# Kernel tuning notes

Hardware: AMD Instinct MI355X
Metric: run time of the kernel (lower is better)

## Reference

```python
import jax, jax.numpy as jnp
import numpy as np

B, N, DIM = 2, 2048, 512
HEADS, DIM_HEAD = 8, 64
INNER = HEADS * DIM_HEAD  # 512
SCALE = DIM_HEAD ** -0.5


def setup_inputs() -> dict:
    key = jax.random.key(0)
    k1, k2, k3, k4, k5 = jax.random.split(key, 5)
    s = 0.02
    return {
        "x1": jax.random.normal(k1, (B, N, DIM), jnp.float32),
        "x2": jax.random.normal(k2, (B, N, DIM), jnp.float32),
        "W_qk": jax.random.normal(k3, (DIM, 2 * INNER), jnp.float32) * s,
        "W_v": jax.random.normal(k4, (DIM, INNER), jnp.float32) * s,
        "W_out": jax.random.normal(k5, (INNER, DIM), jnp.float32) * s,
        "b_out": jnp.zeros((DIM,), jnp.float32),
    }


def _split_heads(t):
    # [b, n, h*d] -> [b, h, n, d]
    b, n, _ = t.shape
    return t.reshape(b, n, HEADS, DIM_HEAD).transpose(0, 2, 1, 3)


def reference(x1, x2, W_qk, W_v, W_out, b_out):
    # to_qk(x1) -> chunk into k, v ; to_v(x2) -> q  (names in orig are swapped)
    kv = x1 @ W_qk                      # [b, n1, 2*inner]
    k, v = jnp.split(kv, 2, axis=-1)
    q = x2 @ W_v                        # [b, n2, inner]
    q, k, v = _split_heads(q), _split_heads(k), _split_heads(v)  # [b,h,n,d]
    dots = jnp.einsum("bhid,bhjd->bhij", q, k) * SCALE  # [b,h,n2,n1]
    attn = jax.nn.softmax(dots, axis=-1)
    out = jnp.einsum("bhij,bhjd->bhid", attn, v)         # [b,h,n2,d]
    out = out.transpose(0, 2, 1, 3).reshape(out.shape[0], out.shape[2], INNER)
    return out @ W_out + b_out          # [b, n2, dim]
```

## Files before the change

### kernel.cpp

```cpp
#include <hip/hip_runtime.h>

typedef short bf16x8 __attribute__((ext_vector_type(8)));
typedef short bf16x4 __attribute__((ext_vector_type(4)));
typedef float f32x4 __attribute__((ext_vector_type(4)));
typedef float f32x16 __attribute__((ext_vector_type(16)));
typedef unsigned short u16;
typedef unsigned int u32;
typedef u16 u16x8 __attribute__((ext_vector_type(8)));
typedef u16 u16x4 __attribute__((ext_vector_type(4)));

#define DEV __device__ __forceinline__

DEV u16 f2bf(float f) {
  unsigned u = __float_as_uint(f);
  u += 0x7fff + ((u >> 16) & 1);
  return (u16)(u >> 16);
}

DEV int pkbf(float lo, float hi) {
  return __builtin_amdgcn_perm(__float_as_uint(hi) + 0x8000u,
                               __float_as_uint(lo) + 0x8000u, 0x07060302u);
}

#define MFMA16(a, b, c) __builtin_amdgcn_mfma_f32_16x16x32_bf16(a, b, c, 0, 0, 0)
#define MFMA3216(a, b, c) __builtin_amdgcn_mfma_f32_32x32x16_bf16(a, b, c, 0, 0, 0)

#if __has_builtin(__builtin_amdgcn_mfma_f32_32x32x8bf16_1k)
#define HAVE_PV8 1
#define PVMFMA(a, b, c) __builtin_amdgcn_mfma_f32_32x32x8bf16_1k(a, b, c, 0, 0, 0)
#else
#define HAVE_PV8 0
#endif

#if __has_builtin(__builtin_amdgcn_exp2f)
#define QSCALE 0.18033688011112042f
#define EXPFN(x) __builtin_amdgcn_exp2f(x)
#else
#define QSCALE 0.125f
#define EXPFN(x) __expf(x)
#endif

#define GLD16(gp, lp)                                                     \
  __builtin_amdgcn_global_load_lds(                                       \
      (const __attribute__((address_space(1))) u32*)(gp),                 \
      (__attribute__((address_space(3))) u32*)(lp), 16, 0, 0)

__global__ __launch_bounds__(256) void wprep(
    const float* __restrict__ Wqk, const float* __restrict__ Wv,
    const float* __restrict__ Wout,
    const float* __restrict__ x1, const float* __restrict__ x2,
    u16* __restrict__ WqkT, u16* __restrict__ WvT, u16* __restrict__ WoutT,
    u16* __restrict__ x1b, u16* __restrict__ x2b) {
  __shared__ float tf[32][33];
  int bx = blockIdx.x, t = threadIdx.x;
  if (bx >= 1024) {
    int id = bx - 1024;
    const float* src = id < 1024 ? x1 : x2;
    u16* dst = id < 1024 ? x1b : x2b;
    long base = (long)(id & 1023) * 2048 + t * 8;
    float4 f0 = *(const float4*)(src + base);
    float4 f1 = *(const float4*)(src + base + 4);
    u16x8 o;
    o[0] = f2bf(f0.x); o[1] = f2bf(f0.y); o[2] = f2bf(f0.z); o[3] = f2bf(f0.w);
    o[4] = f2bf(f1.x); o[5] = f2bf(f1.y); o[6] = f2bf(f1.z); o[7] = f2bf(f1.w);
    *(u16x8*)(dst + base) = o;
    return;
  }
  const float* src; u16* dst; int Ncols; int id;
  if (bx < 512)      { id = bx;       src = Wqk;  dst = WqkT;  Ncols = 1024; }
  else if (bx < 768) { id = bx - 512; src = Wv;   dst = WvT;   Ncols = 512; }
  else               { id = bx - 768; src = Wout; dst = WoutT; Ncols = 512; }
  int tilesPerRow = Ncols >> 5;
  int tr = id / tilesPerRow, tc = id % tilesPerRow;
  int r0 = tr * 32, c0 = tc * 32;
  {
    int r = t >> 3, c4 = (t & 7) * 4;
    float4 v = *(const float4*)(src + (long)(r0 + r) * Ncols + c0 + c4);
    tf[r][c4] = v.x; tf[r][c4 + 1] = v.y; tf[r][c4 + 2] = v.z; tf[r][c4 + 3] = v.w;
  }
  __syncthreads();
  {
    int c = t >> 3, r4 = (t & 7) * 4;
    u16x4 o;
    o[0] = f2bf(tf[r4][c]); o[1] = f2bf(tf[r4 + 1][c]);
    o[2] = f2bf(tf[r4 + 2][c]); o[3] = f2bf(tf[r4 + 3][c]);
    *(u16x4*)(dst + (long)(c0 + c) * 512 + r0 + r4) = o;
  }
}

__global__ __launch_bounds__(256) void qkv_gemm(
    const u16* __restrict__ x1b, const u16* __restrict__ x2b,
    const u16* __restrict__ WqkT, const u16* __restrict__ WvT,
    u16* __restrict__ out_q, u16* __restrict__ out_k, u16* __restrict__ out_vt) {
  __shared__ u16 sA[2][128 * 40];
  __shared__ u16 sB[2][64 * 40];
  int bx = blockIdx.x, t = threadIdx.x;
  bool isQ = bx < 256;
  int bx2 = isQ ? bx : bx - 256;
  const u16* Ap = isQ ? x2b : x1b;
  const u16* BT = isQ ? WvT : WqkT;
  int m0 = (bx2 & 31) * 128, n0 = (bx2 >> 5) * 64;
  int w = t >> 6, l = t & 63, lm = l & 15, lq = l >> 4;

  f32x4 zero = {0.f, 0.f, 0.f, 0.f};
  f32x4 acc[2][4];
#pragma unroll
  for (int i = 0; i < 2; ++i)
#pragma unroll
    for (int j = 0; j < 4; ++j) acc[i][j] = zero;

  int sm = t >> 2;
  int skc = (t & 3) * 8;
  const u16* gA = Ap + (long)(m0 + sm) * 512 + skc;
  const u16* gB = BT + (long)(n0 + sm) * 512 + skc;

  bf16x8 a0 = *(const bf16x8*)(gA);
  bf16x8 a1 = *(const bf16x8*)(gA + 64 * 512);
  bf16x8 b0 = *(const bf16x8*)(gB);
  *(bf16x8*)(sA[0] + sm * 40 + skc) = a0;
  *(bf16x8*)(sA[0] + (sm + 64) * 40 + skc) = a1;
  *(bf16x8*)(sB[0] + sm * 40 + skc) = b0;
  __syncthreads();

  for (int kt = 0; kt < 16; ++kt) {
    int cur = kt & 1;
    if (kt < 15) {
      a0 = *(const bf16x8*)(gA + (kt + 1) * 32);
      a1 = *(const bf16x8*)(gA + 64 * 512 + (kt + 1) * 32);
      b0 = *(const bf16x8*)(gB + (kt + 1) * 32);
    }
    bf16x8 af[2], bfr[4];
    af[0] = *(const bf16x8*)(sA[cur] + (w * 32 + lm) * 40 + lq * 8);
    af[1] = *(const bf16x8*)(sA[cur] + (w * 32 + 16 + lm) * 40 + lq * 8);
#pragma unroll
    for (int s = 0; s < 4; ++s)
      bfr[s] = *(const bf16x8*)(sB[cur] + (s * 16 + lm) * 40 + lq * 8);
#pragma unroll
    for (int ms = 0; ms < 2; ++ms)
#pragma unroll
      for (int s = 0; s < 4; ++s)
        acc[ms][s] = MFMA16(af[ms], bfr[s], acc[ms][s]);
    if (kt < 15) {
      int nxt = 1 - cur;
      *(bf16x8*)(sA[nxt] + sm * 40 + skc) = a0;
      *(bf16x8*)(sA[nxt] + (sm + 64) * 40 + skc) = a1;
      *(bf16x8*)(sB[nxt] + sm * 40 + skc) = b0;
    }
    __syncthreads();
  }

#pragma unroll
  for (int ms = 0; ms < 2; ++ms) {
    int gmBase = m0 + w * 32 + ms * 16 + lq * 4;
#pragma unroll
    for (int s = 0; s < 4; ++s) {
      int gc = n0 + s * 16 + lm;
      int b = gmBase >> 11, n = gmBase & 2047;
      if (isQ) {
#pragma unroll
        for (int r = 0; r < 4; ++r)
          out_q[(((long)(b << 3) + (gc >> 6)) * 2048 + n + r) * 64 + (gc & 63)] =
              f2bf(acc[ms][s][r] * QSCALE);
      } else if (gc < 512) {
#pragma unroll
        for (int r = 0; r < 4; ++r)
          out_k[(((long)(b << 3) + (gc >> 6)) * 2048 + n + r) * 64 + (gc & 63)] =
              f2bf(acc[ms][s][r]);
      } else {
        int c = gc - 512, h = c >> 6, d = c & 63;
        u16x4 vv;
#pragma unroll
        for (int r = 0; r < 4; ++r) vv[r] = f2bf(acc[ms][s][r]);
        *(u16x4*)(out_vt + (((long)(b << 3) + h) * 64 + d) * 2048 + n) = vv;
      }
    }
  }
}

__global__ __launch_bounds__(256, 2) void attn(
    const u16* __restrict__ Q, const u16* __restrict__ K,
    const u16* __restrict__ Vt, u16* __restrict__ O) {
  int id = blockIdx.x;
  int bh = id & 15, qt = id >> 4;
  int b = bh >> 3, h = bh & 7;
  const u16* Kh = K + (long)bh * 2048 * 64;
  const u16* Vh = Vt + (long)bh * 64 * 2048;
  int t = threadIdx.x, w = t >> 6, lane = t & 63, ln = lane & 31, hi = lane >> 5;
  int g = w & 1, kh = w >> 1;

  __shared__ u16 smem[2][2][2][4096];

  bf16x8 qf[4];
  {
    const u16* qp = Q + (long)bh * 2048 * 64 + (long)(qt * 64 + g * 32 + ln) * 64 + hi * 8;
#pragma unroll
    for (int dc = 0; dc < 4; ++dc) qf[dc] = *(const bf16x8*)(qp + dc * 16);
  }

  f32x16 accO[2];
#pragma unroll
  for (int dt = 0; dt < 2; ++dt)
#pragma unroll
    for (int i = 0; i < 16; ++i) accO[dt][i] = 0.f;
  float dacc = 0.f;

  int lrow = lane >> 3;
  int swz = ((lane & 7) ^ lrow) * 8;
  const u16* gKl = Kh + (long)(kh * 1024 + g * 32 + lrow) * 64 + swz;
  const u16* gVl = Vh + (long)(g * 32 + lrow) * 2048 + kh * 1024 + swz;

  auto stage = [&](int jt, int buf) {
    u16* sK = smem[buf][0][kh];
    u16* sV = smem[buf][1][kh];
    const u16* gk = gKl + (long)jt * 4096;
    const u16* gv = gVl + jt * 64;
#pragma unroll
    for (int i = 0; i < 4; ++i) {
      GLD16(gk + i * 512, sK + (g * 32 + i * 8) * 64);
      GLD16(gv + (long)i * 16384, sV + (g * 32 + i * 8) * 64);
    }
  };

  stage(0, 0);
  __syncthreads();

  int swl = ln & 7;
  for (int jt = 0; jt < 16; ++jt) {
    int cur = jt & 1;
    if (jt < 15) stage(jt + 1, cur ^ 1);
    const u16* sKh = smem[cur][0][kh];
    const u16* sVh = smem[cur][1][kh];
#pragma unroll
    for (int kt2 = 0; kt2 < 2; ++kt2) {
      int rowK = (kt2 * 32 + ln) * 64;
      f32x16 st1, st2;
#pragma unroll
      for (int i = 0; i < 16; ++i) { st1[i] = 0.f; st2[i] = 0.f; }
      bf16x8 kf0 = *(const bf16x8*)(sKh + rowK + ((0 * 2 + hi) ^ swl) * 8);
      bf16x8 kf1 = *(const bf16x8*)(sKh + rowK + ((1 * 2 + hi) ^ swl) * 8);
      bf16x8 kf2 = *(const bf16x8*)(sKh + rowK + ((2 * 2 + hi) ^ swl) * 8);
      bf16x8 kf3 = *(const bf16x8*)(sKh + rowK + ((3 * 2 + hi) ^ swl) * 8);
      st1 = MFMA3216(kf0, qf[0], st1);
      st2 = MFMA3216(kf1, qf[1], st2);
      st1 = MFMA3216(kf2, qf[2], st1);
      st2 = MFMA3216(kf3, qf[3], st2);
      float p[16];
#pragma unroll
      for (int i = 0; i < 16; ++i) {
        float e = EXPFN(st1[i] + st2[i]);
        p[i] = e;
        dacc += e;
      }
#if HAVE_PV8
#pragma unroll
      for (int c = 0; c < 4; ++c) {
        union { int2 i2; bf16x4 v; } u;
        u.i2.x = pkbf(p[c * 4 + 0], p[c * 4 + 1]);
        u.i2.y = pkbf(p[c * 4 + 2], p[c * 4 + 3]);
#pragma unroll
        for (int dt = 0; dt < 2; ++dt) {
          bf16x4 vf = *(const bf16x4*)(sVh + (dt * 32 + ln) * 64 +
                                       (((kt2 * 4 + c) ^ swl) * 8) + hi * 4);
          accO[dt] = PVMFMA(vf, u.v, accO[dt]);
        }
      }
#else
#pragma unroll
      for (int c2 = 0; c2 < 2; ++c2) {
        int o0x = pkbf(p[c2 * 8 + 0], p[c2 * 8 + 1]);
        int o0y = pkbf(p[c2 * 8 + 2], p[c2 * 8 + 3]);
        int o1x = pkbf(p[c2 * 8 + 4], p[c2 * 8 + 5]);
        int o1y = pkbf(p[c2 * 8 + 6], p[c2 * 8 + 7]);
        int s0x = __shfl_xor(o0x, 32), s0y = __shfl_xor(o0y, 32);
        int s1x = __shfl_xor(o1x, 32), s1y = __shfl_xor(o1y, 32);
        union { int4 i4; bf16x8 v; } u;
        if (hi) { u.i4.x = s1x; u.i4.y = s1y; u.i4.z = o1x; u.i4.w = o1y; }
        else    { u.i4.x = o0x; u.i4.y = o0y; u.i4.z = s0x; u.i4.w = s0y; }
#pragma unroll
        for (int dt = 0; dt < 2; ++dt) {
          bf16x8 vf = *(const bf16x8*)(sVh + (dt * 32 + ln) * 64 +
                                       (((kt2 * 4 + c2 * 2 + hi) ^ swl) * 8));
          accO[dt] = MFMA3216(vf, u.v, accO[dt]);
        }
      }
#endif
    }
    __syncthreads();
  }

  float* cb = (float*)&smem[0][0][0][0];
  float* base = cb + g * 2112;
  if (kh == 1) {
#pragma unroll
    for (int dt = 0; dt < 2; ++dt)
#pragma unroll
      for (int i = 0; i < 16; ++i)
        base[(dt * 16 + i) * 64 + hi * 32 + ln] = accO[dt][i];
    base[2048 + hi * 32 + ln] = dacc;
  }
  __syncthreads();
  if (kh == 0) {
#pragma unroll
    for (int dt = 0; dt < 2; ++dt)
#pragma unroll
      for (int i = 0; i < 16; ++i)
        accO[dt][i] += base[(dt * 16 + i) * 64 + hi * 32 + ln];
    dacc += base[2048 + hi * 32 + ln];
    dacc += __shfl_xor(dacc, 32);
    float inv = 1.f / dacc;

    u16* Ob = O + ((long)b * 2048 + qt * 64 + g * 32 + ln) * 512 + h * 64;
#pragma unroll
    for (int dt = 0; dt < 2; ++dt)
#pragma unroll
      for (int gq = 0; gq < 4; ++gq) {
        u16x4 o;
#pragma unroll
        for (int rr = 0; rr < 4; ++rr) o[rr] = f2bf(accO[dt][gq * 4 + rr] * inv);
        *(u16x4*)(Ob + dt * 32 + gq * 8 + hi * 4) = o;
      }
  }
}

__global__ __launch_bounds__(128) void out_gemm(
    const u16* __restrict__ A, const u16* __restrict__ BT,
    float* __restrict__ out_f, const float* __restrict__ bias) {
  __shared__ u16 sA[2][64 * 40];
  __shared__ u16 sB[2][32 * 40];
  int t = threadIdx.x, bx = blockIdx.x;
  int m0 = (bx & 63) * 64, n0 = (bx >> 6) * 32;
  int w = t >> 6, l = t & 63, lm = l & 15, lq = l >> 4;

  f32x4 zero = {0.f, 0.f, 0.f, 0.f};
  f32x4 acc[2][2];
#pragma unroll
  for (int i = 0; i < 2; ++i)
#pragma unroll
    for (int j = 0; j < 2; ++j) acc[i][j] = zero;

  int ar = t >> 1, akc = (t & 1) * 16;
  int br = t >> 2, bkc = (t & 3) * 8;
  const u16* gA = A + (long)(m0 + ar) * 512 + akc;
  const u16* gB = BT + (long)(n0 + br) * 512 + bkc;

  bf16x8 a0 = *(const bf16x8*)(gA);
  bf16x8 a1 = *(const bf16x8*)(gA + 8);
  bf16x8 b0 = *(const bf16x8*)(gB);
  *(bf16x8*)(sA[0] + ar * 40 + akc) = a0;
  *(bf16x8*)(sA[0] + ar * 40 + akc + 8) = a1;
  *(bf16x8*)(sB[0] + br * 40 + bkc) = b0;
  __syncthreads();

  for (int kt = 0; kt < 16; ++kt) {
    int cur = kt & 1;
    if (kt < 15) {
      a0 = *(const bf16x8*)(gA + (kt + 1) * 32);
      a1 = *(const bf16x8*)(gA + (kt + 1) * 32 + 8);
      b0 = *(const bf16x8*)(gB + (kt + 1) * 32);
    }
    bf16x8 af[2], bfr[2];
    af[0] = *(const bf16x8*)(sA[cur] + (w * 32 + lm) * 40 + lq * 8);
    af[1] = *(const bf16x8*)(sA[cur] + (w * 32 + 16 + lm) * 40 + lq * 8);
    bfr[0] = *(const bf16x8*)(sB[cur] + (lm)*40 + lq * 8);
    bfr[1] = *(const bf16x8*)(sB[cur] + (16 + lm) * 40 + lq * 8);
#pragma unroll
    for (int ms = 0; ms < 2; ++ms)
#pragma unroll
      for (int s = 0; s < 2; ++s)
        acc[ms][s] = MFMA16(af[ms], bfr[s], acc[ms][s]);
    if (kt < 15) {
      int nxt = 1 - cur;
      *(bf16x8*)(sA[nxt] + ar * 40 + akc) = a0;
      *(bf16x8*)(sA[nxt] + ar * 40 + akc + 8) = a1;
      *(bf16x8*)(sB[nxt] + br * 40 + bkc) = b0;
    }
    __syncthreads();
  }

#pragma unroll
  for (int ms = 0; ms < 2; ++ms) {
    int gmBase = m0 + w * 32 + ms * 16 + lq * 4;
#pragma unroll
    for (int s = 0; s < 2; ++s) {
      int gc = n0 + s * 16 + lm;
      float bv = bias[gc];
#pragma unroll
      for (int r = 0; r < 4; ++r)
        out_f[(long)(gmBase + r) * 512 + gc] = acc[ms][s][r] + bv;
    }
  }
}

extern "C" void kernel_launch(void* const* d_in, const int* in_sizes, int n_in,
                              void* d_out, int out_size, void* d_ws, size_t ws_size,
                              hipStream_t stream) {
  const float* x1 = (const float*)d_in[0];
  const float* x2 = (const float*)d_in[1];
  const float* Wqk = (const float*)d_in[2];
  const float* Wv = (const float*)d_in[3];
  const float* Wout = (const float*)d_in[4];
  const float* bout = (const float*)d_in[5];
  float* out = (float*)d_out;

  u16* ws = (u16*)d_ws;
  const long SZ = 2097152;
  u16* Qw = ws;
  u16* Kw = ws + SZ;
  u16* Vtw = ws + 2 * SZ;
  u16* Ow = ws + 3 * SZ;
  u16* WqkT = ws + 4 * SZ;
  u16* WvT = WqkT + 524288;
  u16* WoutT = WvT + 262144;
  u16* x1b = WoutT + 262144;
  u16* x2b = x1b + SZ;

  wprep<<<3072, 256, 0, stream>>>(Wqk, Wv, Wout, x1, x2, WqkT, WvT, WoutT, x1b, x2b);
  qkv_gemm<<<768, 256, 0, stream>>>(x1b, x2b, WqkT, WvT, Qw, Kw, Vtw);
  attn<<<512, 256, 0, stream>>>(Qw, Kw, Vtw, Ow);
  out_gemm<<<1024, 128, 0, stream>>>(Ow, WoutT, out, bout);
}
```

Before: 126.6 us.

## Use 128x128 GEMM tiles with direct global-to-LDS swizzled loads and MFMA priority hints

The QKV and output projection GEMMs move to 128x128 tiles with a 2x2 wave layout. Operands are staged straight from global memory into LDS through GLD16 with an XOR swizzle instead of register round-trips through padded arrays. The larger tiles raise operand reuse and shrink the grids (384 and 128 blocks), at the cost of fewer blocks to fill the CUs. The attention kernel also gets s_setprio around its MFMA sections and a tree-shaped sum for the softmax denominator.

```diff
diff --git a/kernel.cpp b/kernel.cpp
--- a/kernel.cpp
+++ b/kernel.cpp
@@ -92,70 +92,70 @@
     const u16* __restrict__ x1b, const u16* __restrict__ x2b,
     const u16* __restrict__ WqkT, const u16* __restrict__ WvT,
     u16* __restrict__ out_q, u16* __restrict__ out_k, u16* __restrict__ out_vt) {
-  __shared__ u16 sA[2][128 * 40];
-  __shared__ u16 sB[2][64 * 40];
+  __shared__ u16 sA[2][128 * 32];
+  __shared__ u16 sB[2][128 * 32];
   int bx = blockIdx.x, t = threadIdx.x;
-  bool isQ = bx < 256;
-  int bx2 = isQ ? bx : bx - 256;
+  bool isQ = bx < 128;
+  int bx2 = isQ ? bx : bx - 128;
   const u16* Ap = isQ ? x2b : x1b;
   const u16* BT = isQ ? WvT : WqkT;
-  int m0 = (bx2 & 31) * 128, n0 = (bx2 >> 5) * 64;
+  int m0 = (bx2 & 31) * 128, n0 = (bx2 >> 5) * 128;
   int w = t >> 6, l = t & 63, lm = l & 15, lq = l >> 4;
+  int wr = w >> 1, wc = w & 1;
 
   f32x4 zero = {0.f, 0.f, 0.f, 0.f};
-  f32x4 acc[2][4];
-#pragma unroll
-  for (int i = 0; i < 2; ++i)
+  f32x4 acc[4][4];
+#pragma unroll
+  for (int i = 0; i < 4; ++i)
 #pragma unroll
     for (int j = 0; j < 4; ++j) acc[i][j] = zero;
 
-  int sm = t >> 2;
-  int skc = (t & 3) * 8;
-  const u16* gA = Ap + (long)(m0 + sm) * 512 + skc;
-  const u16* gB = BT + (long)(n0 + sm) * 512 + skc;
-
-  bf16x8 a0 = *(const bf16x8*)(gA);
-  bf16x8 a1 = *(const bf16x8*)(gA + 64 * 512);
-  bf16x8 b0 = *(const bf16x8*)(gB);
-  *(bf16x8*)(sA[0] + sm * 40 + skc) = a0;
-  *(bf16x8*)(sA[0] + (sm + 64) * 40 + skc) = a1;
-  *(bf16x8*)(sB[0] + sm * 40 + skc) = b0;
+  int srow = w * 16 + (l >> 2);
+  int swzk = ((l & 3) ^ ((l >> 3) & 3)) * 8;
+  const u16* gAsrc = Ap + (long)(m0 + srow) * 512 + swzk;
+  const u16* gBsrc = BT + (long)(n0 + srow) * 512 + swzk;
+
+  auto stage = [&](int kt, int buf) {
+    const u16* a0 = gAsrc + kt * 32;
+    const u16* b0 = gBsrc + kt * 32;
+    GLD16(a0,            sA[buf] + w * 512);
+    GLD16(a0 + 64 * 512, sA[buf] + 2048 + w * 512);
+    GLD16(b0,            sB[buf] + w * 512);
+    GLD16(b0 + 64 * 512, sB[buf] + 2048 + w * 512);
+  };
+
+  stage(0, 0);
   __syncthreads();
+
+  int rchunk = (lq ^ ((lm >> 1) & 3)) * 8;
+  int frA = (wr * 64 + lm) * 32 + rchunk;
+  int frB = (wc * 64 + lm) * 32 + rchunk;
 
   for (int kt = 0; kt < 16; ++kt) {
     int cur = kt & 1;
-    if (kt < 15) {
-      a0 = *(const bf16x8*)(gA + (kt + 1) * 32);
-      a1 = *(const bf16x8*)(gA + 64 * 512 + (kt + 1) * 32);
-      b0 = *(const bf16x8*)(gB + (kt + 1) * 32);
-    }
-    bf16x8 af[2], bfr[4];
-    af[0] = *(const bf16x8*)(sA[cur] + (w * 32 + lm) * 40 + lq * 8);
-    af[1] = *(const bf16x8*)(sA[cur] + (w * 32 + 16 + lm) * 40 + lq * 8);
+    if (kt < 15) stage(kt + 1, cur ^ 1);
+    bf16x8 af[4], bfr[4];
+#pragma unroll
+    for (int ms = 0; ms < 4; ++ms)
+      af[ms] = *(const bf16x8*)(sA[cur] + frA + ms * 512);
 #pragma unroll
     for (int s = 0; s < 4; ++s)
-      bfr[s] = *(const bf16x8*)(sB[cur] + (s * 16 + lm) * 40 + lq * 8);
-#pragma unroll
-    for (int ms = 0; ms < 2; ++ms)
+      bfr[s] = *(const bf16x8*)(sB[cur] + frB + s * 512);
+#pragma unroll
+    for (int ms = 0; ms < 4; ++ms)
 #pragma unroll
       for (int s = 0; s < 4; ++s)
         acc[ms][s] = MFMA16(af[ms], bfr[s], acc[ms][s]);
-    if (kt < 15) {
-      int nxt = 1 - cur;
-      *(bf16x8*)(sA[nxt] + sm * 40 + skc) = a0;
-      *(bf16x8*)(sA[nxt] + (sm + 64) * 40 + skc) = a1;
-      *(bf16x8*)(sB[nxt] + sm * 40 + skc) = b0;
-    }
     __syncthreads();
   }
 
 #pragma unroll
-  for (int ms = 0; ms < 2; ++ms) {
-    int gmBase = m0 + w * 32 + ms * 16 + lq * 4;
+  for (int ms = 0; ms < 4; ++ms) {
+    int gmBase = m0 + wr * 64 + ms * 16 + lq * 4;
+    int b = gmBase >> 11, n = gmBase & 2047;
 #pragma unroll
     for (int s = 0; s < 4; ++s) {
-      int gc = n0 + s * 16 + lm;
-      int b = gmBase >> 11, n = gmBase & 2047;
+      int gc = n0 + wc * 64 + s * 16 + lm;
       if (isQ) {
 #pragma unroll
         for (int r = 0; r < 4; ++r)
@@ -240,18 +240,22 @@
       bf16x8 kf1 = *(const bf16x8*)(sKh + rowK + ((1 * 2 + hi) ^ swl) * 8);
       bf16x8 kf2 = *(const bf16x8*)(sKh + rowK + ((2 * 2 + hi) ^ swl) * 8);
       bf16x8 kf3 = *(const bf16x8*)(sKh + rowK + ((3 * 2 + hi) ^ swl) * 8);
+      __builtin_amdgcn_s_setprio(1);
       st1 = MFMA3216(kf0, qf[0], st1);
       st2 = MFMA3216(kf1, qf[1], st2);
       st1 = MFMA3216(kf2, qf[2], st1);
       st2 = MFMA3216(kf3, qf[3], st2);
+      __builtin_amdgcn_s_setprio(0);
       float p[16];
 #pragma unroll
-      for (int i = 0; i < 16; ++i) {
-        float e = EXPFN(st1[i] + st2[i]);
-        p[i] = e;
-        dacc += e;
-      }
+      for (int i = 0; i < 16; ++i) p[i] = EXPFN(st1[i] + st2[i]);
+      float q0 = (p[0] + p[1]) + (p[2] + p[3]);
+      float q1 = (p[4] + p[5]) + (p[6] + p[7]);
+      float q2 = (p[8] + p[9]) + (p[10] + p[11]);
+      float q3 = (p[12] + p[13]) + (p[14] + p[15]);
+      dacc += (q0 + q1) + (q2 + q3);
 #if HAVE_PV8
+      __builtin_amdgcn_s_setprio(1);
 #pragma unroll
       for (int c = 0; c < 4; ++c) {
         union { int2 i2; bf16x4 v; } u;
@@ -264,7 +268,9 @@
           accO[dt] = PVMFMA(vf, u.v, accO[dt]);
         }
       }
+      __builtin_amdgcn_s_setprio(0);
 #else
+      __builtin_amdgcn_s_setprio(1);
 #pragma unroll
       for (int c2 = 0; c2 < 2; ++c2) {
         int o0x = pkbf(p[c2 * 8 + 0], p[c2 * 8 + 1]);
@@ -283,6 +289,7 @@
           accO[dt] = MFMA3216(vf, u.v, accO[dt]);
         }
       }
+      __builtin_amdgcn_s_setprio(0);
 #endif
     }
     __syncthreads();
@@ -322,71 +329,72 @@
   }
 }
 
-__global__ __launch_bounds__(128) void out_gemm(
+__global__ __launch_bounds__(256) void out_gemm(
     const u16* __restrict__ A, const u16* __restrict__ BT,
     float* __restrict__ out_f, const float* __restrict__ bias) {
-  __shared__ u16 sA[2][64 * 40];
-  __shared__ u16 sB[2][32 * 40];
-  int t = threadIdx.x, bx = blockIdx.x;
-  int m0 = (bx & 63) * 64, n0 = (bx >> 6) * 32;
+  __shared__ u16 sA[2][128 * 32];
+  __shared__ u16 sB[2][128 * 32];
+  int bx = blockIdx.x, t = threadIdx.x;
+  int m0 = (bx & 31) * 128, n0 = (bx >> 5) * 128;
   int w = t >> 6, l = t & 63, lm = l & 15, lq = l >> 4;
+  int wr = w >> 1, wc = w & 1;
 
   f32x4 zero = {0.f, 0.f, 0.f, 0.f};
-  f32x4 acc[2][2];
-#pragma unroll
-  for (int i = 0; i < 2; ++i)
-#pragma unroll
-    for (int j = 0; j < 2; ++j) acc[i][j] = zero;
-
-  int ar = t >> 1, akc = (t & 1) * 16;
-  int br = t >> 2, bkc = (t & 3) * 8;
-  const u16* gA = A + (long)(m0 + ar) * 512 + akc;
-  const u16* gB = BT + (long)(n0 + br) * 512 + bkc;
-
-  bf16x8 a0 = *(const bf16x8*)(gA);
-  bf16x8 a1 = *(const bf16x8*)(gA + 8);
-  bf16x8 b0 = *(const bf16x8*)(gB);
-  *(bf16x8*)(sA[0] + ar * 40 + akc) = a0;
-  *(bf16x8*)(sA[0] + ar * 40 + akc + 8) = a1;
-  *(bf16x8*)(sB[0] + br * 40 + bkc) = b0;
+  f32x4 acc[4][4];
+#pragma unroll
+  for (int i = 0; i < 4; ++i)
+#pragma unroll
+    for (int j = 0; j < 4; ++j) acc[i][j] = zero;
+
+  int srow = w * 16 + (l >> 2);
+  int swzk = ((l & 3) ^ ((l >> 3) & 3)) * 8;
+  const u16* gAsrc = A + (long)(m0 + srow) * 512 + swzk;
+  const u16* gBsrc = BT + (long)(n0 + srow) * 512 + swzk;
+
+  auto stage = [&](int kt, int buf) {
+    const u16* a0 = gAsrc + kt * 32;
+    const u16* b0 = gBsrc + kt * 32;
+    GLD16(a0,            sA[buf] + w * 512);
+    GLD16(a0 + 64 * 512, sA[buf] + 2048 + w * 512);
+    GLD16(b0,            sB[buf] + w * 512);
+    GLD16(b0 + 64 * 512, sB[buf] + 2048 + w * 512);
+  };
+
+  stage(0, 0);
   __syncthreads();
+
+  int rchunk = (lq ^ ((lm >> 1) & 3)) * 8;
+  int frA = (wr * 64 + lm) * 32 + rchunk;
+  int frB = (wc * 64 + lm) * 32 + rchunk;
 
   for (int kt = 0; kt < 16; ++kt) {
     int cur = kt & 1;
-    if (kt < 15) {
-      a0 = *(const bf16x8*)(gA + (kt + 1) * 32);
-      a1 = *(const bf16x8*)(gA + (kt + 1) * 32 + 8);
-      b0 = *(const bf16x8*)(gB + (kt + 1) * 32);
-    }
-    bf16x8 af[2], bfr[2];
-    af[0] = *(const bf16x8*)(sA[cur] + (w * 32 + lm) * 40 + lq * 8);
-    af[1] = *(const bf16x8*)(sA[cur] + (w * 32 + 16 + lm) * 40 + lq * 8);
-    bfr[0] = *(const bf16x8*)(sB[cur] + (lm)*40 + lq * 8);
-    bfr[1] = *(const bf16x8*)(sB[cur] + (16 + lm) * 40 + lq * 8);
-#pragma unroll
-    for (int ms = 0; ms < 2; ++ms)
-#pragma unroll
-      for (int s = 0; s < 2; ++s)
+    if (kt < 15) stage(kt + 1, cur ^ 1);
+    bf16x8 af[4], bfr[4];
+#pragma unroll
+    for (int ms = 0; ms < 4; ++ms)
+      af[ms] = *(const bf16x8*)(sA[cur] + frA + ms * 512);
+#pragma unroll
+    for (int s = 0; s < 4; ++s)
+      bfr[s] = *(const bf16x8*)(sB[cur] + frB + s * 512);
+#pragma unroll
+    for (int ms = 0; ms < 4; ++ms)
+#pragma unroll
+      for (int s = 0; s < 4; ++s)
         acc[ms][s] = MFMA16(af[ms], bfr[s], acc[ms][s]);
-    if (kt < 15) {
-      int nxt = 1 - cur;
-      *(bf16x8*)(sA[nxt] + ar * 40 + akc) = a0;
-      *(bf16x8*)(sA[nxt] + ar * 40 + akc + 8) = a1;
-      *(bf16x8*)(sB[nxt] + br * 40 + bkc) = b0;
-    }
     __syncthreads();
   }
 
 #pragma unroll
-  for (int ms = 0; ms < 2; ++ms) {
-    int gmBase = m0 + w * 32 + ms * 16 + lq * 4;
-#pragma unroll
-    for (int s = 0; s < 2; ++s) {
-      int gc = n0 + s * 16 + lm;
+  for (int ms = 0; ms < 4; ++ms) {
+    int gm = m0 + wr * 64 + ms * 16 + lq * 4;
+#pragma unroll
+    for (int s = 0; s < 4; ++s) {
+      int gc = n0 + wc * 64 + s * 16 + lm;
       float bv = bias[gc];
 #pragma unroll
       for (int r = 0; r < 4; ++r)
-        out_f[(long)(gmBase + r) * 512 + gc] = acc[ms][s][r] + bv;
+        out_f[(long)(gm + r) * 512 + gc] = acc[ms][s][r] + bv;
     }
   }
 }
@@ -415,7 +423,7 @@
   u16* x2b = x1b + SZ;
 
   wprep<<<3072, 256, 0, stream>>>(Wqk, Wv, Wout, x1, x2, WqkT, WvT, WoutT, x1b, x2b);
-  qkv_gemm<<<768, 256, 0, stream>>>(x1b, x2b, WqkT, WvT, Qw, Kw, Vtw);
+  qkv_gemm<<<384, 256, 0, stream>>>(x1b, x2b, WqkT, WvT, Qw, Kw, Vtw);
   attn<<<512, 256, 0, stream>>>(Qw, Kw, Vtw, Ow);
-  out_gemm<<<1024, 128, 0, stream>>>(Ow, WoutT, out, bout);
-}
+  out_gemm<<<128, 256, 0, stream>>>(Ow, WoutT, out, bout);
+}
```

New measurement: 132.4 us. 4.6% more time.
